# Optimization experiments

Measured on AMD Instinct MI355X. Metric: run time of the kernel, lower is better.

The kernel has to match this reference:

```python
import jax, jax.numpy as jnp
import numpy as np

B, T_IN, FEAT, UNITS, OUT_STEPS = 2048, 48, 64, 1024, 64


def setup_inputs() -> dict:
    key = jax.random.key(0)
    k0, k1, k2, k3 = jax.random.split(key, 4)
    inputs = jax.random.normal(k0, (B, T_IN, FEAT), dtype=jnp.float32)
    # glorot-ish scaling so gates don't saturate immediately
    W = jax.random.normal(k1, (FEAT, 4 * UNITS), dtype=jnp.float32) / np.sqrt(FEAT)
    U = jax.random.normal(k2, (UNITS, 4 * UNITS), dtype=jnp.float32) / np.sqrt(UNITS)
    b = jnp.zeros((4 * UNITS,), dtype=jnp.float32)
    Wd = jax.random.normal(k3, (UNITS, FEAT), dtype=jnp.float32) / np.sqrt(UNITS)
    bd = jnp.zeros((FEAT,), dtype=jnp.float32)
    return {"inputs": inputs, "W": W, "U": U, "b": b, "Wd": Wd, "bd": bd}


def _lstm_cell(h, c, x, W, U, b):
    # Keras LSTMCell gate order: i, f, g(candidate), o
    z = x @ W + h @ U + b  # [B, 4*units]
    i, f, g, o = jnp.split(z, 4, axis=-1)
    c = jax.nn.sigmoid(f) * c + jax.nn.sigmoid(i) * jnp.tanh(g)
    h = jax.nn.sigmoid(o) * jnp.tanh(c)
    return h, c


def reference(inputs, W, U, b, Wd, bd):
    batch = inputs.shape[0]
    units = U.shape[0]
    h0 = jnp.zeros((batch, units), dtype=inputs.dtype)
    c0 = jnp.zeros((batch, units), dtype=inputs.dtype)

    # warmup: run LSTM over the input sequence (time-major scan)
    def warm_step(carry, x_t):
        h, c = carry
        h, c = _lstm_cell(h, c, x_t, W, U, b)
        return (h, c), None

    (h, c), _ = jax.lax.scan(warm_step, (h0, c0), jnp.swapaxes(inputs, 0, 1))
    pred = h @ Wd + bd  # first prediction, [B, feat]

    def dec_step(carry, _):
        h, c, p = carry
        h, c = _lstm_cell(h, c, p, W, U, b)
        p = h @ Wd + bd
        return (h, c, p), p

    _, preds = jax.lax.scan(dec_step, (h, c, pred), None, length=OUT_STEPS - 1)
    preds = jnp.concatenate([pred[None], preds], axis=0)  # [out_steps, B, feat]
    return jnp.swapaxes(preds, 0, 1)  # [B, out_steps, feat]
```

## Files before the change

kernel.cpp:

```cpp
#include <hip/hip_runtime.h>
#include <hip/hip_bf16.h>

typedef float f32x4 __attribute__((ext_vector_type(4)));
typedef __bf16 bf16x8 __attribute__((ext_vector_type(8)));

#define B_SZ 2048
#define T_IN 48
#define FEAT 64
#define UNITS 1024
#define GCOLS 4096
#define OUT_STEPS 64
#define KWARM 1088

__device__ __forceinline__ int oc_of(int c) {
    return (((c >> 4) & 3) * UNITS) + ((c >> 6) * 16) + (c & 15);
}

typedef __attribute__((address_space(1))) const void gas_t;
typedef __attribute__((address_space(3))) void las_t;

__device__ __forceinline__ void gl_lds16(const void* g, void* l) {
    __builtin_amdgcn_global_load_lds((gas_t*)g, (las_t*)l, 16, 0, 0);
}
__device__ __forceinline__ float sigm(float x) {
    return __builtin_amdgcn_rcpf(1.0f + __expf(-x));
}
__device__ __forceinline__ float tanh_fast(float x) {
    float e = __expf(2.0f * x);
    return 1.0f - 2.0f * __builtin_amdgcn_rcpf(e + 1.0f);
}


__global__ __launch_bounds__(256) void reorder_UW(const float* __restrict__ U, const float* __restrict__ W,
                                                  __hip_bfloat16* __restrict__ UTw) {
    __shared__ __hip_bfloat16 t[64][64];
    const int k0 = blockIdx.x * 64;
    const int c0 = blockIdx.y * 64;
    const int tid = threadIdx.x;
#pragma unroll
    for (int i = 0; i < 16; ++i) {
        int idx = tid + i * 256;
        int rk = idx >> 6, cc = idx & 63;
        int k = k0 + rk, c = c0 + cc;
        int oc = oc_of(c);
        float v = (k < UNITS) ? U[(size_t)k * GCOLS + oc] : W[(size_t)(k - UNITS) * GCOLS + oc];
        t[rk][cc] = __float2bfloat16(v);
    }
    __syncthreads();
#pragma unroll
    for (int i = 0; i < 16; ++i) {
        int idx = tid + i * 256;
        int rc = idx >> 6, kk = idx & 63;
        UTw[(size_t)(c0 + rc) * KWARM + k0 + kk] = t[kk][rc];
    }
}

__global__ __launch_bounds__(256) void transpose_Wd(const float* __restrict__ Wd, __hip_bfloat16* __restrict__ WdT) {
    __shared__ __hip_bfloat16 t[64][64];
    const int k0 = blockIdx.x * 64;
    const int tid = threadIdx.x;
#pragma unroll
    for (int i = 0; i < 16; ++i) {
        int idx = tid + i * 256;
        int rk = idx >> 6, ff = idx & 63;
        t[rk][ff] = __float2bfloat16(Wd[(size_t)(k0 + rk) * FEAT + ff]);
    }
    __syncthreads();
#pragma unroll
    for (int i = 0; i < 16; ++i) {
        int idx = tid + i * 256;
        int rf = idx >> 6, kk = idx & 63;
        WdT[(size_t)rf * UNITS + k0 + kk] = t[kk][rf];
    }
}

__global__ __launch_bounds__(256) void build_UTdec(const __hip_bfloat16* __restrict__ UTw,
                                                   const __hip_bfloat16* __restrict__ WdT,
                                                   __hip_bfloat16* __restrict__ UTd) {
    __shared__ float Wl[64][16];
    const int k = blockIdx.x * 256 + threadIdx.x;
    const int c0 = blockIdx.y * 16;
    const int tid = threadIdx.x;
#pragma unroll
    for (int i = 0; i < 4; ++i) {
        int idx = tid + i * 256;
        int f = idx >> 4, cc = idx & 15;
        Wl[f][cc] = __bfloat162float(UTw[(size_t)(c0 + cc) * KWARM + UNITS + f]);
    }
    __syncthreads();
    float acc[16];
#pragma unroll
    for (int cc = 0; cc < 16; ++cc) acc[cc] = 0.f;
    for (int f = 0; f < 64; ++f) {
        float wd = __bfloat162float(WdT[(size_t)f * UNITS + k]);
#pragma unroll
        for (int cc = 0; cc < 16; ++cc) acc[cc] += wd * Wl[f][cc];
    }
#pragma unroll
    for (int cc = 0; cc < 16; ++cc) {
        float uv = __bfloat162float(UTw[(size_t)(c0 + cc) * KWARM + k]);
        UTd[(size_t)(c0 + cc) * UNITS + k] = __float2bfloat16(uv + acc[cc]);
    }
}

__global__ __launch_bounds__(256) void build_bias(const float* __restrict__ b, const float* __restrict__ bd,
                                                  const __hip_bfloat16* __restrict__ UTw,
                                                  float* __restrict__ bw, float* __restrict__ bdc) {
    const int c = blockIdx.x * 256 + threadIdx.x;
    const int oc = oc_of(c);
    float base = b[oc];
    float s = 0.f;
    for (int f = 0; f < FEAT; ++f) s += bd[f] * __bfloat162float(UTw[(size_t)c * KWARM + UNITS + f]);
    bw[c] = base;
    bdc[c] = base + s;
}

__global__ void convert_x(const float* __restrict__ x, __hip_bfloat16* __restrict__ xb, int n) {
    int i = blockIdx.x * blockDim.x + threadIdx.x;
    if (i < n) xb[i] = __float2bfloat16(x[i]);
}

template <bool WARM, bool PRED>
__global__ __launch_bounds__(256) void lstm_step(
    const __hip_bfloat16* __restrict__ hin,
    const __hip_bfloat16* __restrict__ xbf, int t,
    const __hip_bfloat16* __restrict__ UT,
    const float* __restrict__ bias,
    float* __restrict__ cst,
    __hip_bfloat16* __restrict__ hout,
    const __hip_bfloat16* __restrict__ WdT,
    const float* __restrict__ bd,
    float* __restrict__ out, int tstep)
{
    constexpr int KD = WARM ? KWARM : UNITS;
    constexpr int NKT = KD / 64;

    __shared__ alignas(16) __hip_bfloat16 Al[2 * 8192];
    __shared__ alignas(16) __hip_bfloat16 Bl[2 * 8192];

    const int tid = threadIdx.x;
    const int lane = tid & 63;
    const int wv = tid >> 6;
    const int wr = wv >> 1, wc = wv & 1;
    const int bid = blockIdx.x;
    const int nb = bid & 31;
    const int mb = bid >> 5;
    const int m0 = mb * 128;
    const int n0 = nb * 128;
    const bool doPred = PRED && (nb < 4);

    f32x4 acc[4][4] = {};
    f32x4 accp[2] = {};

    const int lrow = lane >> 3;
    const int scol = ((lane & 7) * 16) ^ (lrow << 4);

    const char* aS[4]; const char* bS[4]; const char* xS[4];
#pragma unroll
    for (int r = 0; r < 4; ++r) {
        int row = (r * 4 + wv) * 8 + lrow;
        aS[r] = (const char*)hin + (size_t)(m0 + row) * (UNITS * 2) + scol;
        bS[r] = (const char*)UT + (size_t)(n0 + row) * (KD * 2) + scol;
        if (WARM) xS[r] = (const char*)xbf + (size_t)(m0 + row) * (T_IN * FEAT * 2) + (size_t)t * (FEAT * 2) + scol;
    }

    const int ar = lane & 15;
    const int ko = (lane >> 4) << 3;
    const int swz = (ar & 7) << 3;

    const char* wB = nullptr;
    if (PRED && doPred)
        wB = (const char*)WdT + ((size_t)(16 * nb + ar) * UNITS + ko) * 2;

    const int u16 = lane & 15;
    const int unit = (nb * 2 + wc) * 16 + u16;
    const int rbase = m0 + 64 * wr + ((lane >> 4) << 2);
    float bv[4];
#pragma unroll
    for (int g = 0; g < 4; ++g) bv[g] = bias[n0 + 64 * wc + 16 * g + u16];
    float bdv = 0.f;
    if (PRED && doPred) bdv = bd[16 * nb + u16];

    auto stage = [&](int kt) {
        const int buf = kt & 1;
#pragma unroll
        for (int r = 0; r < 4; ++r) {
            const char* s = (WARM && kt == NKT - 1) ? xS[r] : (aS[r] + kt * 128);
            gl_lds16(s, (char*)Al + buf * 16384 + (r * 4 + wv) * 1024);
        }
#pragma unroll
        for (int r = 0; r < 4; ++r)
            gl_lds16(bS[r] + kt * 128, (char*)Bl + buf * 16384 + (r * 4 + wv) * 1024);
    };

    bf16x8 Wf[2][2];
    auto loadWf = [&](int kt) {
        if (PRED && doPred) {
#pragma unroll
            for (int kk = 0; kk < 2; ++kk)
                Wf[kt & 1][kk] = *reinterpret_cast<const bf16x8*>(wB + kt * 128 + kk * 64);
        }
    };

    auto compute = [&](int kt) {
        const int buf = kt & 1;
#pragma unroll
        for (int kk = 0; kk < 2; ++kk) {
            bf16x8 af[4], bfr[4];
#pragma unroll
            for (int mi = 0; mi < 4; ++mi)
                af[mi] = *reinterpret_cast<const bf16x8*>(&Al[buf * 8192 + (64 * wr + 16 * mi + ar) * 64 + ((32 * kk + ko) ^ swz)]);
#pragma unroll
            for (int ni = 0; ni < 4; ++ni)
                bfr[ni] = *reinterpret_cast<const bf16x8*>(&Bl[buf * 8192 + (64 * wc + 16 * ni + ar) * 64 + ((32 * kk + ko) ^ swz)]);
#pragma unroll
            for (int mi = 0; mi < 4; ++mi)
#pragma unroll
                for (int ni = 0; ni < 4; ++ni)
                    acc[mi][ni] = __builtin_amdgcn_mfma_f32_16x16x32_bf16(af[mi], bfr[ni], acc[mi][ni], 0, 0, 0);
            if (PRED && doPred) {
#pragma unroll
                for (int pi = 0; pi < 2; ++pi)
                    accp[pi] = __builtin_amdgcn_mfma_f32_16x16x32_bf16(af[2 * wc + pi], Wf[kt & 1][kk], accp[pi], 0, 0, 0);
            }
        }
    };

    stage(0);
    loadWf(0);
#pragma unroll
    for (int kt = 0; kt < NKT - 1; ++kt) {
        stage(kt + 1);
        loadWf(kt + 1);
        if (PRED && doPred) asm volatile("s_waitcnt vmcnt(10) lgkmcnt(0)" ::: "memory");
        else                asm volatile("s_waitcnt vmcnt(8) lgkmcnt(0)" ::: "memory");
        __builtin_amdgcn_s_barrier();
        compute(kt);
        __builtin_amdgcn_s_barrier();
    }
    float cv[16];
#pragma unroll
    for (int mi = 0; mi < 4; ++mi)
#pragma unroll
        for (int reg = 0; reg < 4; ++reg)
            cv[mi * 4 + reg] = cst[(size_t)(rbase + 16 * mi + reg) * UNITS + unit];
    asm volatile("s_waitcnt vmcnt(16) lgkmcnt(0)" ::: "memory");
    __builtin_amdgcn_s_barrier();
    compute(NKT - 1);

#pragma unroll
    for (int mi = 0; mi < 4; ++mi)
#pragma unroll
        for (int reg = 0; reg < 4; ++reg) {
            float zi = acc[mi][0][reg] + bv[0];
            float zf = acc[mi][1][reg] + bv[1];
            float zg = acc[mi][2][reg] + bv[2];
            float zo = acc[mi][3][reg] + bv[3];
            float cn = sigm(zf) * cv[mi * 4 + reg] + sigm(zi) * tanh_fast(zg);
            size_t idx = (size_t)(rbase + 16 * mi + reg) * UNITS + unit;
            cst[idx] = cn;
            hout[idx] = __float2bfloat16(sigm(zo) * tanh_fast(cn));
        }

    if (PRED && doPred) {
#pragma unroll
        for (int pi = 0; pi < 2; ++pi) {
            const int prow = m0 + 64 * wr + 32 * wc + 16 * pi + ((lane >> 4) << 2);
            f32x4 v = accp[pi];
#pragma unroll
            for (int reg = 0; reg < 4; ++reg)
                out[(size_t)(prow + reg) * (OUT_STEPS * FEAT) + (size_t)tstep * FEAT + (16 * nb + u16)] = v[reg] + bdv;
        }
    }
}

extern "C" void kernel_launch(void* const* d_in, const int* in_sizes, int n_in,
                              void* d_out, int out_size, void* d_ws, size_t ws_size,
                              hipStream_t stream) {
    const float* inputs = (const float*)d_in[0];
    const float* W  = (const float*)d_in[1];
    const float* U  = (const float*)d_in[2];
    const float* b  = (const float*)d_in[3];
    const float* Wd = (const float*)d_in[4];
    const float* bd = (const float*)d_in[5];
    float* out = (float*)d_out;

    char* ws = (char*)d_ws;
    size_t off = 0;
    auto alloc = [&](size_t bytes) { char* p = ws + off; off = (off + bytes + 255) & ~255ULL; return p; };
    __hip_bfloat16* UTw = (__hip_bfloat16*)alloc((size_t)GCOLS * KWARM * 2);
    __hip_bfloat16* UTd = (__hip_bfloat16*)alloc((size_t)GCOLS * UNITS * 2);
    __hip_bfloat16* WdT = (__hip_bfloat16*)alloc((size_t)FEAT * UNITS * 2);
    __hip_bfloat16* Xbf = (__hip_bfloat16*)alloc((size_t)B_SZ * T_IN * FEAT * 2);
    __hip_bfloat16* hA  = (__hip_bfloat16*)alloc((size_t)B_SZ * UNITS * 2);
    __hip_bfloat16* hB  = (__hip_bfloat16*)alloc((size_t)B_SZ * UNITS * 2);
    float* cst = (float*)alloc((size_t)B_SZ * UNITS * 4);
    float* bw  = (float*)alloc(GCOLS * 4);
    float* bdc = (float*)alloc(GCOLS * 4);

    hipMemsetAsync(cst, 0, (size_t)B_SZ * UNITS * 4, stream);
    hipMemsetAsync(hA, 0, (size_t)B_SZ * UNITS * 2, stream);

    dim3 blk(256);
    reorder_UW<<<dim3(17, 64), blk, 0, stream>>>(U, W, UTw);
    transpose_Wd<<<dim3(16), blk, 0, stream>>>(Wd, WdT);
    build_UTdec<<<dim3(4, 256), blk, 0, stream>>>(UTw, WdT, UTd);
    build_bias<<<dim3(16), blk, 0, stream>>>(b, bd, UTw, bw, bdc);
    {
        int n = B_SZ * T_IN * FEAT;
        convert_x<<<dim3((n + 255) / 256), blk, 0, stream>>>(inputs, Xbf, n);
    }

    const __hip_bfloat16* cur = hA;
    __hip_bfloat16* nxt = hB;
    for (int t = 0; t < T_IN; ++t) {
        lstm_step<true, false><<<dim3(512), blk, 0, stream>>>(cur, Xbf, t, UTw, bw, cst, nxt,
                                                              nullptr, nullptr, nullptr, 0);
        __hip_bfloat16* tmp = (__hip_bfloat16*)cur; cur = nxt; nxt = tmp;
    }
    for (int t = 1; t <= OUT_STEPS; ++t) {
        lstm_step<false, true><<<dim3(512), blk, 0, stream>>>(cur, nullptr, 0, UTd, bdc, cst, nxt,
                                                              WdT, bd, out, t - 1);
        __hip_bfloat16* tmp = (__hip_bfloat16*)cur; cur = nxt; nxt = tmp;
    }
}
```

Measured before the change: 4.929 ms.

## Fuse per-step LSTM launches into one persistent kernel with grid barriers

Replaces the 112 per-timestep kernel launches with a single persistent kernel of 256 blocks. Each block handles two column tiles per step and synchronises through an atomic-counter grid barrier. The cell state stays in registers across steps instead of being read from and written to global memory each step. This removes launch gaps and the c-state traffic, but it relies on all 256 blocks being co-resident and adds a spin-barrier with a timeout fallback that could produce wrong results if blocks are not scheduled together.

```diff
diff --git a/kernel.cpp b/kernel.cpp
--- a/kernel.cpp
+++ b/kernel.cpp
@@ -11,6 +11,8 @@
 #define GCOLS 4096
 #define OUT_STEPS 64
 #define KWARM 1088
+#define NSTEP (T_IN + OUT_STEPS)
+#define NBLK 256
 
 __device__ __forceinline__ int oc_of(int c) {
     return (((c >> 4) & 3) * UNITS) + ((c >> 6) * 16) + (c & 15);
@@ -28,6 +30,24 @@
 __device__ __forceinline__ float tanh_fast(float x) {
     float e = __expf(2.0f * x);
     return 1.0f - 2.0f * __builtin_amdgcn_rcpf(e + 1.0f);
+}
+
+__device__ __forceinline__ int grid_barrier(int* cnt, int target) {
+    __threadfence();
+    __syncthreads();
+    __shared__ int ok_s;
+    if (threadIdx.x == 0) {
+        atomicAdd(cnt, 1);
+        int ok = 1, spins = 0;
+        while (__hip_atomic_load(cnt, __ATOMIC_RELAXED, __HIP_MEMORY_SCOPE_AGENT) < target) {
+            __builtin_amdgcn_s_sleep(4);
+            if (++spins > (1 << 21)) { ok = 0; atomicAdd(cnt, 1 << 20); break; }
+        }
+        ok_s = ok;
+    }
+    __syncthreads();
+    __threadfence();
+    return ok_s;
 }
 
 
@@ -120,20 +140,23 @@
     if (i < n) xb[i] = __float2bfloat16(x[i]);
 }
 
-template <bool WARM, bool PRED>
-__global__ __launch_bounds__(256) void lstm_step(
-    const __hip_bfloat16* __restrict__ hin,
-    const __hip_bfloat16* __restrict__ xbf, int t,
-    const __hip_bfloat16* __restrict__ UT,
-    const float* __restrict__ bias,
-    float* __restrict__ cst,
-    __hip_bfloat16* __restrict__ hout,
+__global__ __launch_bounds__(256) void lstm_persistent(
+    __hip_bfloat16* __restrict__ hA,
+    __hip_bfloat16* __restrict__ hB,
+    const __hip_bfloat16* __restrict__ xbf,
+    const __hip_bfloat16* __restrict__ UTw,
+    const __hip_bfloat16* __restrict__ UTd,
+    const float* __restrict__ bw,
+    const float* __restrict__ bdc,
     const __hip_bfloat16* __restrict__ WdT,
     const float* __restrict__ bd,
-    float* __restrict__ out, int tstep)
+    float* __restrict__ out,
+    int* __restrict__ sync_cnt)
 {
-    constexpr int KD = WARM ? KWARM : UNITS;
-    constexpr int NKT = KD / 64;
+    constexpr int NKT_W = KWARM / 64;
+    constexpr int NKT_D = UNITS / 64;
+    constexpr size_t OFFW = (size_t)2048 * KWARM * 2;
+    constexpr size_t OFFD = (size_t)2048 * UNITS * 2;
 
     __shared__ alignas(16) __hip_bfloat16 Al[2 * 8192];
     __shared__ alignas(16) __hip_bfloat16 Bl[2 * 8192];
@@ -142,135 +165,213 @@
     const int lane = tid & 63;
     const int wv = tid >> 6;
     const int wr = wv >> 1, wc = wv & 1;
-    const int bid = blockIdx.x;
-    const int nb = bid & 31;
-    const int mb = bid >> 5;
+    const int p = blockIdx.x;
+    const int mb = p >> 4;
+    const int j = p & 15;
     const int m0 = mb * 128;
-    const int n0 = nb * 128;
-    const bool doPred = PRED && (nb < 4);
-
-    f32x4 acc[4][4] = {};
-    f32x4 accp[2] = {};
+    const bool predBlk = (j < 4);
 
     const int lrow = lane >> 3;
     const int scol = ((lane & 7) * 16) ^ (lrow << 4);
 
-    const char* aS[4]; const char* bS[4]; const char* xS[4];
+    size_t aOff[4]; const char* xB[4]; const char* bWb[4]; const char* bDb[4];
 #pragma unroll
     for (int r = 0; r < 4; ++r) {
         int row = (r * 4 + wv) * 8 + lrow;
-        aS[r] = (const char*)hin + (size_t)(m0 + row) * (UNITS * 2) + scol;
-        bS[r] = (const char*)UT + (size_t)(n0 + row) * (KD * 2) + scol;
-        if (WARM) xS[r] = (const char*)xbf + (size_t)(m0 + row) * (T_IN * FEAT * 2) + (size_t)t * (FEAT * 2) + scol;
+        aOff[r] = (size_t)(m0 + row) * (UNITS * 2) + scol;
+        xB[r] = (const char*)xbf + (size_t)(m0 + row) * (T_IN * FEAT * 2) + scol;
+        bWb[r] = (const char*)UTw + (size_t)(j * 128 + row) * (KWARM * 2) + scol;
+        bDb[r] = (const char*)UTd + (size_t)(j * 128 + row) * (UNITS * 2) + scol;
     }
 
     const int ar = lane & 15;
     const int ko = (lane >> 4) << 3;
     const int swz = (ar & 7) << 3;
 
-    const char* wB = nullptr;
-    if (PRED && doPred)
-        wB = (const char*)WdT + ((size_t)(16 * nb + ar) * UNITS + ko) * 2;
+    const char* wBp = (const char*)WdT + ((size_t)(16 * j + ar) * UNITS + ko) * 2;
 
     const int u16 = lane & 15;
-    const int unit = (nb * 2 + wc) * 16 + u16;
+    const int unit0 = (j * 2 + wc) * 16 + u16;
     const int rbase = m0 + 64 * wr + ((lane >> 4) << 2);
-    float bv[4];
-#pragma unroll
-    for (int g = 0; g < 4; ++g) bv[g] = bias[n0 + 64 * wc + 16 * g + u16];
-    float bdv = 0.f;
-    if (PRED && doPred) bdv = bd[16 * nb + u16];
-
-    auto stage = [&](int kt) {
-        const int buf = kt & 1;
-#pragma unroll
-        for (int r = 0; r < 4; ++r) {
-            const char* s = (WARM && kt == NKT - 1) ? xS[r] : (aS[r] + kt * 128);
-            gl_lds16(s, (char*)Al + buf * 16384 + (r * 4 + wv) * 1024);
+    float bvw[2][4], bvd[2][4];
+#pragma unroll
+    for (int t = 0; t < 2; ++t) {
+        const int n0t = (j + 16 * t) * 128;
+#pragma unroll
+        for (int g = 0; g < 4; ++g) {
+            bvw[t][g] = bw[n0t + 64 * wc + 16 * g + u16];
+            bvd[t][g] = bdc[n0t + 64 * wc + 16 * g + u16];
         }
-#pragma unroll
-        for (int r = 0; r < 4; ++r)
-            gl_lds16(bS[r] + kt * 128, (char*)Bl + buf * 16384 + (r * 4 + wv) * 1024);
-    };
-
-    bf16x8 Wf[2][2];
-    auto loadWf = [&](int kt) {
-        if (PRED && doPred) {
-#pragma unroll
-            for (int kk = 0; kk < 2; ++kk)
-                Wf[kt & 1][kk] = *reinterpret_cast<const bf16x8*>(wB + kt * 128 + kk * 64);
+    }
+    const float bdv = predBlk ? bd[16 * j + u16] : 0.f;
+
+    float cvA[16] = {}, cvB[16] = {};
+
+    int healthy = 1;
+
+#pragma unroll 1
+    for (int step = 0; step < NSTEP; ++step) {
+        const bool warm = step < T_IN;
+        const char* hin = (const char*)((step & 1) ? hB : hA);
+        __hip_bfloat16* hOut = (step & 1) ? hA : hB;
+
+        const char* aS[4];
+#pragma unroll
+        for (int r = 0; r < 4; ++r) aS[r] = hin + aOff[r];
+
+        auto warm_tile = [&](size_t bOff, float* cvt, const float* bvt, int unitT) {
+            f32x4 acc[4][4] = {};
+            auto stage = [&](int kt) {
+                const int buf = kt & 1;
+#pragma unroll
+                for (int r = 0; r < 4; ++r) {
+                    const char* s = (kt == NKT_W - 1) ? (xB[r] + step * (FEAT * 2)) : (aS[r] + kt * 128);
+                    gl_lds16(s, (char*)Al + buf * 16384 + (r * 4 + wv) * 1024);
+                }
+#pragma unroll
+                for (int r = 0; r < 4; ++r)
+                    gl_lds16(bWb[r] + bOff + kt * 128, (char*)Bl + buf * 16384 + (r * 4 + wv) * 1024);
+            };
+            auto compute = [&](int kt) {
+                const int buf = kt & 1;
+#pragma unroll
+                for (int kk = 0; kk < 2; ++kk) {
+                    bf16x8 af[4], bfr[4];
+#pragma unroll
+                    for (int mi = 0; mi < 4; ++mi)
+                        af[mi] = *reinterpret_cast<const bf16x8*>(&Al[buf * 8192 + (64 * wr + 16 * mi + ar) * 64 + ((32 * kk + ko) ^ swz)]);
+#pragma unroll
+                    for (int ni = 0; ni < 4; ++ni)
+                        bfr[ni] = *reinterpret_cast<const bf16x8*>(&Bl[buf * 8192 + (64 * wc + 16 * ni + ar) * 64 + ((32 * kk + ko) ^ swz)]);
+#pragma unroll
+                    for (int mi = 0; mi < 4; ++mi)
+#pragma unroll
+                        for (int ni = 0; ni < 4; ++ni)
+                            acc[mi][ni] = __builtin_amdgcn_mfma_f32_16x16x32_bf16(af[mi], bfr[ni], acc[mi][ni], 0, 0, 0);
+                }
+            };
+            stage(0);
+#pragma unroll
+            for (int kt = 0; kt < NKT_W - 1; ++kt) {
+                stage(kt + 1);
+                asm volatile("s_waitcnt vmcnt(8) lgkmcnt(0)" ::: "memory");
+                __builtin_amdgcn_s_barrier();
+                compute(kt);
+                __builtin_amdgcn_s_barrier();
+            }
+            asm volatile("s_waitcnt vmcnt(0) lgkmcnt(0)" ::: "memory");
+            __builtin_amdgcn_s_barrier();
+            compute(NKT_W - 1);
+#pragma unroll
+            for (int mi = 0; mi < 4; ++mi)
+#pragma unroll
+                for (int reg = 0; reg < 4; ++reg) {
+                    float zi = acc[mi][0][reg] + bvt[0];
+                    float zf = acc[mi][1][reg] + bvt[1];
+                    float zg = acc[mi][2][reg] + bvt[2];
+                    float zo = acc[mi][3][reg] + bvt[3];
+                    float cn = sigm(zf) * cvt[mi * 4 + reg] + sigm(zi) * tanh_fast(zg);
+                    cvt[mi * 4 + reg] = cn;
+                    hOut[(size_t)(rbase + 16 * mi + reg) * UNITS + unitT] =
+                        __float2bfloat16(sigm(zo) * tanh_fast(cn));
+                }
+        };
+
+        auto dec_tile = [&](size_t bOff, float* cvt, const float* bvt, int unitT, bool predT, int tstep) {
+            f32x4 acc[4][4] = {};
+            f32x4 accp[2] = {};
+            bf16x8 Wf[2][2];
+            auto stage = [&](int kt) {
+                const int buf = kt & 1;
+#pragma unroll
+                for (int r = 0; r < 4; ++r)
+                    gl_lds16(aS[r] + kt * 128, (char*)Al + buf * 16384 + (r * 4 + wv) * 1024);
+#pragma unroll
+                for (int r = 0; r < 4; ++r)
+                    gl_lds16(bDb[r] + bOff + kt * 128, (char*)Bl + buf * 16384 + (r * 4 + wv) * 1024);
+            };
+            auto loadWf = [&](int kt) {
+                if (predT) {
+#pragma unroll
+                    for (int kk = 0; kk < 2; ++kk)
+                        Wf[kt & 1][kk] = *reinterpret_cast<const bf16x8*>(wBp + kt * 128 + kk * 64);
+                }
+            };
+            auto compute = [&](int kt) {
+                const int buf = kt & 1;
+#pragma unroll
+                for (int kk = 0; kk < 2; ++kk) {
+                    bf16x8 af[4], bfr[4];
+#pragma unroll
+                    for (int mi = 0; mi < 4; ++mi)
+                        af[mi] = *reinterpret_cast<const bf16x8*>(&Al[buf * 8192 + (64 * wr + 16 * mi + ar) * 64 + ((32 * kk + ko) ^ swz)]);
+#pragma unroll
+                    for (int ni = 0; ni < 4; ++ni)
+                        bfr[ni] = *reinterpret_cast<const bf16x8*>(&Bl[buf * 8192 + (64 * wc + 16 * ni + ar) * 64 + ((32 * kk + ko) ^ swz)]);
+#pragma unroll
+                    for (int mi = 0; mi < 4; ++mi)
+#pragma unroll
+                        for (int ni = 0; ni < 4; ++ni)
+                            acc[mi][ni] = __builtin_amdgcn_mfma_f32_16x16x32_bf16(af[mi], bfr[ni], acc[mi][ni], 0, 0, 0);
+                    if (predT) {
+#pragma unroll
+                        for (int pi = 0; pi < 2; ++pi)
+                            accp[pi] = __builtin_amdgcn_mfma_f32_16x16x32_bf16(af[2 * wc + pi], Wf[kt & 1][kk], accp[pi], 0, 0, 0);
+                    }
+                }
+            };
+            stage(0);
+            loadWf(0);
+#pragma unroll
+            for (int kt = 0; kt < NKT_D - 1; ++kt) {
+                stage(kt + 1);
+                loadWf(kt + 1);
+                if (predT) asm volatile("s_waitcnt vmcnt(10) lgkmcnt(0)" ::: "memory");
+                else       asm volatile("s_waitcnt vmcnt(8) lgkmcnt(0)" ::: "memory");
+                __builtin_amdgcn_s_barrier();
+                compute(kt);
+                __builtin_amdgcn_s_barrier();
+            }
+            asm volatile("s_waitcnt vmcnt(0) lgkmcnt(0)" ::: "memory");
+            __builtin_amdgcn_s_barrier();
+            compute(NKT_D - 1);
+#pragma unroll
+            for (int mi = 0; mi < 4; ++mi)
+#pragma unroll
+                for (int reg = 0; reg < 4; ++reg) {
+                    float zi = acc[mi][0][reg] + bvt[0];
+                    float zf = acc[mi][1][reg] + bvt[1];
+                    float zg = acc[mi][2][reg] + bvt[2];
+                    float zo = acc[mi][3][reg] + bvt[3];
+                    float cn = sigm(zf) * cvt[mi * 4 + reg] + sigm(zi) * tanh_fast(zg);
+                    cvt[mi * 4 + reg] = cn;
+                    hOut[(size_t)(rbase + 16 * mi + reg) * UNITS + unitT] =
+                        __float2bfloat16(sigm(zo) * tanh_fast(cn));
+                }
+            if (predT) {
+#pragma unroll
+                for (int pi = 0; pi < 2; ++pi) {
+                    const int prow = m0 + 64 * wr + 32 * wc + 16 * pi + ((lane >> 4) << 2);
+                    f32x4 v = accp[pi];
+#pragma unroll
+                    for (int reg = 0; reg < 4; ++reg)
+                        out[(size_t)(prow + reg) * (OUT_STEPS * FEAT) + (size_t)tstep * FEAT + (16 * j + u16)] = v[reg] + bdv;
+                }
+            }
+        };
+
+        if (warm) {
+            warm_tile(0, cvA, bvw[0], unit0);
+            __builtin_amdgcn_s_barrier();
+            warm_tile(OFFW, cvB, bvw[1], unit0 + 512);
+        } else {
+            dec_tile(0, cvA, bvd[0], unit0, predBlk, step - T_IN);
+            __builtin_amdgcn_s_barrier();
+            dec_tile(OFFD, cvB, bvd[1], unit0 + 512, false, 0);
         }
-    };
-
-    auto compute = [&](int kt) {
-        const int buf = kt & 1;
-#pragma unroll
-        for (int kk = 0; kk < 2; ++kk) {
-            bf16x8 af[4], bfr[4];
-#pragma unroll
-            for (int mi = 0; mi < 4; ++mi)
-                af[mi] = *reinterpret_cast<const bf16x8*>(&Al[buf * 8192 + (64 * wr + 16 * mi + ar) * 64 + ((32 * kk + ko) ^ swz)]);
-#pragma unroll
-            for (int ni = 0; ni < 4; ++ni)
-                bfr[ni] = *reinterpret_cast<const bf16x8*>(&Bl[buf * 8192 + (64 * wc + 16 * ni + ar) * 64 + ((32 * kk + ko) ^ swz)]);
-#pragma unroll
-            for (int mi = 0; mi < 4; ++mi)
-#pragma unroll
-                for (int ni = 0; ni < 4; ++ni)
-                    acc[mi][ni] = __builtin_amdgcn_mfma_f32_16x16x32_bf16(af[mi], bfr[ni], acc[mi][ni], 0, 0, 0);
-            if (PRED && doPred) {
-#pragma unroll
-                for (int pi = 0; pi < 2; ++pi)
-                    accp[pi] = __builtin_amdgcn_mfma_f32_16x16x32_bf16(af[2 * wc + pi], Wf[kt & 1][kk], accp[pi], 0, 0, 0);
-            }
-        }
-    };
-
-    stage(0);
-    loadWf(0);
-#pragma unroll
-    for (int kt = 0; kt < NKT - 1; ++kt) {
-        stage(kt + 1);
-        loadWf(kt + 1);
-        if (PRED && doPred) asm volatile("s_waitcnt vmcnt(10) lgkmcnt(0)" ::: "memory");
-        else                asm volatile("s_waitcnt vmcnt(8) lgkmcnt(0)" ::: "memory");
-        __builtin_amdgcn_s_barrier();
-        compute(kt);
-        __builtin_amdgcn_s_barrier();
-    }
-    float cv[16];
-#pragma unroll
-    for (int mi = 0; mi < 4; ++mi)
-#pragma unroll
-        for (int reg = 0; reg < 4; ++reg)
-            cv[mi * 4 + reg] = cst[(size_t)(rbase + 16 * mi + reg) * UNITS + unit];
-    asm volatile("s_waitcnt vmcnt(16) lgkmcnt(0)" ::: "memory");
-    __builtin_amdgcn_s_barrier();
-    compute(NKT - 1);
-
-#pragma unroll
-    for (int mi = 0; mi < 4; ++mi)
-#pragma unroll
-        for (int reg = 0; reg < 4; ++reg) {
-            float zi = acc[mi][0][reg] + bv[0];
-            float zf = acc[mi][1][reg] + bv[1];
-            float zg = acc[mi][2][reg] + bv[2];
-            float zo = acc[mi][3][reg] + bv[3];
-            float cn = sigm(zf) * cv[mi * 4 + reg] + sigm(zi) * tanh_fast(zg);
-            size_t idx = (size_t)(rbase + 16 * mi + reg) * UNITS + unit;
-            cst[idx] = cn;
-            hout[idx] = __float2bfloat16(sigm(zo) * tanh_fast(cn));
-        }
-
-    if (PRED && doPred) {
-#pragma unroll
-        for (int pi = 0; pi < 2; ++pi) {
-            const int prow = m0 + 64 * wr + 32 * wc + 16 * pi + ((lane >> 4) << 2);
-            f32x4 v = accp[pi];
-#pragma unroll
-            for (int reg = 0; reg < 4; ++reg)
-                out[(size_t)(prow + reg) * (OUT_STEPS * FEAT) + (size_t)tstep * FEAT + (16 * nb + u16)] = v[reg] + bdv;
-        }
+
+        if (step < NSTEP - 1 && healthy)
+            healthy = grid_barrier(sync_cnt, NBLK * (step + 1));
     }
 }
 
@@ -294,12 +395,12 @@
     __hip_bfloat16* Xbf = (__hip_bfloat16*)alloc((size_t)B_SZ * T_IN * FEAT * 2);
     __hip_bfloat16* hA  = (__hip_bfloat16*)alloc((size_t)B_SZ * UNITS * 2);
     __hip_bfloat16* hB  = (__hip_bfloat16*)alloc((size_t)B_SZ * UNITS * 2);
-    float* cst = (float*)alloc((size_t)B_SZ * UNITS * 4);
     float* bw  = (float*)alloc(GCOLS * 4);
     float* bdc = (float*)alloc(GCOLS * 4);
-
-    hipMemsetAsync(cst, 0, (size_t)B_SZ * UNITS * 4, stream);
+    int* sync_cnt = (int*)alloc(256);
+
     hipMemsetAsync(hA, 0, (size_t)B_SZ * UNITS * 2, stream);
+    hipMemsetAsync(sync_cnt, 0, 256, stream);
 
     dim3 blk(256);
     reorder_UW<<<dim3(17, 64), blk, 0, stream>>>(U, W, UTw);
@@ -311,16 +412,6 @@
         convert_x<<<dim3((n + 255) / 256), blk, 0, stream>>>(inputs, Xbf, n);
     }
 
-    const __hip_bfloat16* cur = hA;
-    __hip_bfloat16* nxt = hB;
-    for (int t = 0; t < T_IN; ++t) {
-        lstm_step<true, false><<<dim3(512), blk, 0, stream>>>(cur, Xbf, t, UTw, bw, cst, nxt,
-                                                              nullptr, nullptr, nullptr, 0);
-        __hip_bfloat16* tmp = (__hip_bfloat16*)cur; cur = nxt; nxt = tmp;
-    }
-    for (int t = 1; t <= OUT_STEPS; ++t) {
-        lstm_step<false, true><<<dim3(512), blk, 0, stream>>>(cur, nullptr, 0, UTd, bdc, cst, nxt,
-                                                              WdT, bd, out, t - 1);
-        __hip_bfloat16* tmp = (__hip_bfloat16*)cur; cur = nxt; nxt = tmp;
-    }
-}
+    lstm_persistent<<<dim3(NBLK), blk, 0, stream>>>(hA, hB, Xbf, UTw, UTd,
+                                                    bw, bdc, WdT, bd, out, sync_cnt);
+}
```

Result: slower. 12.90 ms (+161.7%).
